# Kernel tuning notes

Hardware: AMD Instinct MI355X
Metric: run time of the kernel (lower is better)

Reference implementation:

```python
import jax, jax.numpy as jnp
import numpy as np

N = 8192        # batch rows
D = 1024        # final_dim (power of 2, == init_dim so padding = 0)
STACK = 4       # nbr_stack
SIGMA = 1.0


def _hadamard(n):
    H = np.array([[1.0]], dtype=np.float32)
    while H.shape[0] < n:
        H = np.block([[H, H], [H, -H]])
    return H


def setup_inputs() -> dict:
    key = jax.random.key(0)
    x = jax.random.normal(key, (N, D), dtype=jnp.float32)
    rs = np.random.RandomState(0)
    # B: random signs (diag), shape (STACK, D)
    B = jnp.asarray(rs.choice([-1.0, 1.0], size=(STACK, D)).astype(np.float32))
    # G: gaussian diag, flattened to (STACK*D,)
    G2 = rs.randn(STACK, D).astype(np.float32)
    G = jnp.asarray(G2.reshape(STACK * D))
    # S: chi-like scaling normalized by per-stack norm of G, flattened
    G_norm = np.linalg.norm(G2, axis=1, keepdims=True)
    S2 = (np.abs(rs.randn(STACK, D)).astype(np.float32) * np.sqrt(D)) / G_norm
    S = jnp.asarray(S2.reshape(STACK * D).astype(np.float32))
    # H: dense Walsh-Hadamard matrix (D, D), +-1 entries (non-trainable constant)
    H = jnp.asarray(_hadamard(D))
    # P: per-stack permutation with stack offsets, gathered along feature axis
    P = jnp.asarray(np.concatenate([rs.permutation(D) + i * D for i in range(STACK)]).astype(np.int32))
    bias = jnp.zeros((2 * STACK * D,), dtype=jnp.float32)
    return {"x": x, "B": B, "G": G, "S": S, "bias": bias, "H": H, "P": P}


def reference(x, B, G, S, bias, H, P):
    n = x.shape[0]
    # padding = final_dim - init_dim = 0 here; pad kept for faithfulness
    xp = jnp.pad(x.reshape(-1, D), ((0, 0), (0, 0)))
    # diag B then Hadamard matmul: [n, STACK, D]
    h = xp[:, None, :] * B
    h = jnp.einsum('nsd,de->nse', h, H).reshape(n, STACK * D)
    # permutation gather, diag G
    h = h[:, P] * G
    # second Hadamard matmul
    h = jnp.einsum('nsd,de->nse', h.reshape(n, STACK, D), H).reshape(n, STACK * D)
    # scale by 1/(sigma*sqrt(D)) and diag S
    h = (1.0 / (SIGMA * np.sqrt(D))) * h * S
    # cos/sin random-feature activation
    out = np.sqrt(1.0 / D).astype(np.float32) * jnp.concatenate([jnp.cos(h), jnp.sin(h)], axis=1)
    out = out + bias
    return out
```

## Files before the change

### kernel.cpp

```cpp
#include <hip/hip_runtime.h>
#include <math.h>


#define FF_D 1024
#define FF_STACK 4
#define FF_NT 256

__device__ __forceinline__ int swz(int e) { return e ^ (((e >> 6) & 7) << 2); }

#define STAGE_BIT(vv, m) { \
    _Pragma("unroll") \
    for (int i_ = 0; i_ < 16; ++i_) \
        if (!(i_ & (m))) { \
            float s_ = vv[i_] + vv[i_ | (m)]; \
            float d_ = vv[i_] - vv[i_ | (m)]; \
            vv[i_] = s_; vv[i_ | (m)] = d_; \
        } \
}

__global__ __launch_bounds__(FF_NT) void fastfood_kernel(
    const float* __restrict__ x,
    const float* __restrict__ Bs,
    const float* __restrict__ G,
    const float* __restrict__ S,
    const float* __restrict__ bias,
    const int*   __restrict__ P,
    float* __restrict__ out)
{
    __shared__ float lds[FF_STACK * FF_D];
    const int lane = threadIdx.x & 63;
    const int s    = threadIdx.x >> 6;
    const int row  = blockIdx.x;
    const int sb   = s << 10;
    float* wl = lds + sb;

    const int eB = (lane & 3) | ((lane & 60) << 4);
    const float kout = 0.03125f;
    const float karg = 0.03125f * 0.15915494309f;

    float v[16];

    #pragma unroll
    for (int q = 0; q < 4; ++q) {
        const float4 t  = *(const float4*)&x[((long long)row << 10) + (q << 8) + (lane << 2)];
        const float4 b4 = *(const float4*)&Bs[sb + (q << 8) + (lane << 2)];
        v[4*q+0] = t.x * b4.x; v[4*q+1] = t.y * b4.y;
        v[4*q+2] = t.z * b4.z; v[4*q+3] = t.w * b4.w;
    }

    STAGE_BIT(v, 1) STAGE_BIT(v, 2) STAGE_BIT(v, 4) STAGE_BIT(v, 8)
    #pragma unroll
    for (int q = 0; q < 4; ++q)
        *(float4*)&wl[swz((q << 8) | (lane << 2))] =
            make_float4(v[4*q], v[4*q+1], v[4*q+2], v[4*q+3]);
    __builtin_amdgcn_wave_barrier();
    #pragma unroll
    for (int r = 0; r < 16; ++r) v[r] = wl[swz(eB | (r << 2))];
    STAGE_BIT(v, 1) STAGE_BIT(v, 2) STAGE_BIT(v, 4) STAGE_BIT(v, 8)
    __builtin_amdgcn_wave_barrier();
    #pragma unroll
    for (int r = 0; r < 16; ++r) wl[swz(eB | (r << 2))] = v[r];
    __builtin_amdgcn_wave_barrier();
    #pragma unroll
    for (int q = 0; q < 4; ++q) {
        const float4 t = *(const float4*)&wl[swz(((lane & 15) << 2) | (q << 6) | ((lane & 48) << 4))];
        v[4*q+0] = t.x; v[4*q+1] = t.y; v[4*q+2] = t.z; v[4*q+3] = t.w;
    }
    STAGE_BIT(v, 4) STAGE_BIT(v, 8)

    __builtin_amdgcn_wave_barrier();
    #pragma unroll
    for (int q = 0; q < 4; ++q)
        *(float4*)&wl[swz(((lane & 15) << 2) | (q << 6) | ((lane & 48) << 4))] =
            make_float4(v[4*q], v[4*q+1], v[4*q+2], v[4*q+3]);
    __builtin_amdgcn_wave_barrier();
    #pragma unroll
    for (int q = 0; q < 4; ++q) {
        const int jb = sb + (q << 8) + (lane << 2);
        const int4   p4 = *(const int4*)&P[jb];
        const float4 g4 = *(const float4*)&G[jb];
        v[4*q+0] = wl[swz(p4.x & (FF_D - 1))] * g4.x;
        v[4*q+1] = wl[swz(p4.y & (FF_D - 1))] * g4.y;
        v[4*q+2] = wl[swz(p4.z & (FF_D - 1))] * g4.z;
        v[4*q+3] = wl[swz(p4.w & (FF_D - 1))] * g4.w;
    }

    STAGE_BIT(v, 1) STAGE_BIT(v, 2) STAGE_BIT(v, 4) STAGE_BIT(v, 8)
    __builtin_amdgcn_wave_barrier();
    #pragma unroll
    for (int q = 0; q < 4; ++q)
        *(float4*)&wl[swz((q << 8) | (lane << 2))] =
            make_float4(v[4*q], v[4*q+1], v[4*q+2], v[4*q+3]);
    __builtin_amdgcn_wave_barrier();
    #pragma unroll
    for (int r = 0; r < 16; ++r) v[r] = wl[swz(eB | (r << 2))];
    STAGE_BIT(v, 1) STAGE_BIT(v, 2) STAGE_BIT(v, 4) STAGE_BIT(v, 8)
    __builtin_amdgcn_wave_barrier();
    #pragma unroll
    for (int r = 0; r < 16; ++r) wl[swz(eB | (r << 2))] = v[r];
    __builtin_amdgcn_wave_barrier();
    #pragma unroll
    for (int q = 0; q < 4; ++q) {
        const float4 t = *(const float4*)&wl[swz(((lane & 15) << 2) | (q << 6) | ((lane & 48) << 4))];
        v[4*q+0] = t.x; v[4*q+1] = t.y; v[4*q+2] = t.z; v[4*q+3] = t.w;
    }
    STAGE_BIT(v, 4) STAGE_BIT(v, 8)

    const long long obase = ((long long)row << 13);
    #pragma unroll
    for (int q = 0; q < 4; ++q) {
        const int e0 = ((lane & 15) << 2) | (q << 6) | ((lane & 48) << 4);
        const int j  = sb + e0;
        const float4 s4  = *(const float4*)&S[j];
        const float4 bc4 = *(const float4*)&bias[j];
        const float4 bs4 = *(const float4*)&bias[FF_STACK * FF_D + j];
        float4 oc, os;
        {
            const float tr = __builtin_amdgcn_fractf(v[4*q+0] * (s4.x * karg));
            oc.x = __builtin_amdgcn_cosf(tr) * kout + bc4.x;
            os.x = __builtin_amdgcn_sinf(tr) * kout + bs4.x;
        }
        {
            const float tr = __builtin_amdgcn_fractf(v[4*q+1] * (s4.y * karg));
            oc.y = __builtin_amdgcn_cosf(tr) * kout + bc4.y;
            os.y = __builtin_amdgcn_sinf(tr) * kout + bs4.y;
        }
        {
            const float tr = __builtin_amdgcn_fractf(v[4*q+2] * (s4.z * karg));
            oc.z = __builtin_amdgcn_cosf(tr) * kout + bc4.z;
            os.z = __builtin_amdgcn_sinf(tr) * kout + bs4.z;
        }
        {
            const float tr = __builtin_amdgcn_fractf(v[4*q+3] * (s4.w * karg));
            oc.w = __builtin_amdgcn_cosf(tr) * kout + bc4.w;
            os.w = __builtin_amdgcn_sinf(tr) * kout + bs4.w;
        }
        *(float4*)&out[obase + j] = oc;
        *(float4*)&out[obase + FF_STACK * FF_D + j] = os;
    }
}

extern "C" void kernel_launch(void* const* d_in, const int* in_sizes, int n_in,
                              void* d_out, int out_size, void* d_ws, size_t ws_size,
                              hipStream_t stream) {
    const float* x    = (const float*)d_in[0];
    const float* B    = (const float*)d_in[1];
    const float* G    = (const float*)d_in[2];
    const float* S    = (const float*)d_in[3];
    const float* bias = (const float*)d_in[4];
    const int*   P    = (const int*)d_in[6];
    float* out = (float*)d_out;

    const int n_rows = in_sizes[0] / FF_D;
    fastfood_kernel<<<n_rows, FF_NT, 0, stream>>>(x, B, G, S, bias, P, out);
}
```

Measured before the change: 321.1 us.

## Replace LDS transposes in Hadamard transform with cross-lane swizzle butterflies

The LDS store/load transposes used for the upper butterfly stages of each 1024-point Walsh-Hadamard transform are replaced. Those stages now run as cross-lane exchanges (ds_swizzle for lane distances 1-16, shfl_xor for 32), with a per-lane sign applied through an FMA. LDS is kept only for the permutation gather, now without address swizzling. This removes LDS round trips and wave barriers but issues 16 swizzle ops per stage across 6 stages, and the unswizzled gather may hit more bank conflicts.

```diff
diff --git a/kernel.cpp b/kernel.cpp
--- a/kernel.cpp
+++ b/kernel.cpp
@@ -1,12 +1,12 @@
 #include <hip/hip_runtime.h>
-#include <math.h>
 
 
 #define FF_D 1024
 #define FF_STACK 4
 #define FF_NT 256
 
-__device__ __forceinline__ int swz(int e) { return e ^ (((e >> 6) & 7) << 2); }
+#define SWZF(vf, OFF) \
+    __int_as_float(__builtin_amdgcn_ds_swizzle(__float_as_int(vf), (OFF)))
 
 #define STAGE_BIT(vv, m) { \
     _Pragma("unroll") \
@@ -16,6 +16,32 @@
             float d_ = vv[i_] - vv[i_ | (m)]; \
             vv[i_] = s_; vv[i_ | (m)] = d_; \
         } \
+}
+
+#define STAGE_SWZ(vv, OFF, sgn) { \
+    float p_[16]; \
+    _Pragma("unroll") \
+    for (int i_ = 0; i_ < 16; ++i_) p_[i_] = SWZF(vv[i_], OFF); \
+    _Pragma("unroll") \
+    for (int i_ = 0; i_ < 16; ++i_) vv[i_] = __builtin_fmaf(sgn, vv[i_], p_[i_]); \
+}
+
+#define STAGE_X32(vv, sgn) { \
+    float p_[16]; \
+    _Pragma("unroll") \
+    for (int i_ = 0; i_ < 16; ++i_) p_[i_] = __shfl_xor(vv[i_], 32, 64); \
+    _Pragma("unroll") \
+    for (int i_ = 0; i_ < 16; ++i_) vv[i_] = __builtin_fmaf(sgn, vv[i_], p_[i_]); \
+}
+
+#define FWHT10(vv) { \
+    STAGE_BIT(vv, 1) STAGE_BIT(vv, 2) STAGE_BIT(vv, 4) STAGE_BIT(vv, 8) \
+    STAGE_SWZ(vv, 0x041F, sg1)   \
+    STAGE_SWZ(vv, 0x081F, sg2)   \
+    STAGE_SWZ(vv, 0x101F, sg4)   \
+    STAGE_SWZ(vv, 0x201F, sg8)   \
+    STAGE_SWZ(vv, 0x401F, sg16)  \
+    STAGE_X32(vv, sg32)          \
 }
 
 __global__ __launch_bounds__(FF_NT) void fastfood_kernel(
@@ -34,7 +60,13 @@
     const int sb   = s << 10;
     float* wl = lds + sb;
 
-    const int eB = (lane & 3) | ((lane & 60) << 4);
+    const float sg1  = (lane & 1)  ? -1.0f : 1.0f;
+    const float sg2  = (lane & 2)  ? -1.0f : 1.0f;
+    const float sg4  = (lane & 4)  ? -1.0f : 1.0f;
+    const float sg8  = (lane & 8)  ? -1.0f : 1.0f;
+    const float sg16 = (lane & 16) ? -1.0f : 1.0f;
+    const float sg32 = (lane & 32) ? -1.0f : 1.0f;
+
     const float kout = 0.03125f;
     const float karg = 0.03125f * 0.15915494309f;
 
@@ -48,30 +80,11 @@
         v[4*q+2] = t.z * b4.z; v[4*q+3] = t.w * b4.w;
     }
 
-    STAGE_BIT(v, 1) STAGE_BIT(v, 2) STAGE_BIT(v, 4) STAGE_BIT(v, 8)
+    FWHT10(v)
+
     #pragma unroll
     for (int q = 0; q < 4; ++q)
-        *(float4*)&wl[swz((q << 8) | (lane << 2))] =
-            make_float4(v[4*q], v[4*q+1], v[4*q+2], v[4*q+3]);
-    __builtin_amdgcn_wave_barrier();
-    #pragma unroll
-    for (int r = 0; r < 16; ++r) v[r] = wl[swz(eB | (r << 2))];
-    STAGE_BIT(v, 1) STAGE_BIT(v, 2) STAGE_BIT(v, 4) STAGE_BIT(v, 8)
-    __builtin_amdgcn_wave_barrier();
-    #pragma unroll
-    for (int r = 0; r < 16; ++r) wl[swz(eB | (r << 2))] = v[r];
-    __builtin_amdgcn_wave_barrier();
-    #pragma unroll
-    for (int q = 0; q < 4; ++q) {
-        const float4 t = *(const float4*)&wl[swz(((lane & 15) << 2) | (q << 6) | ((lane & 48) << 4))];
-        v[4*q+0] = t.x; v[4*q+1] = t.y; v[4*q+2] = t.z; v[4*q+3] = t.w;
-    }
-    STAGE_BIT(v, 4) STAGE_BIT(v, 8)
-
-    __builtin_amdgcn_wave_barrier();
-    #pragma unroll
-    for (int q = 0; q < 4; ++q)
-        *(float4*)&wl[swz(((lane & 15) << 2) | (q << 6) | ((lane & 48) << 4))] =
+        *(float4*)&wl[(q << 8) | (lane << 2)] =
             make_float4(v[4*q], v[4*q+1], v[4*q+2], v[4*q+3]);
     __builtin_amdgcn_wave_barrier();
     #pragma unroll
@@ -79,38 +92,18 @@
         const int jb = sb + (q << 8) + (lane << 2);
         const int4   p4 = *(const int4*)&P[jb];
         const float4 g4 = *(const float4*)&G[jb];
-        v[4*q+0] = wl[swz(p4.x & (FF_D - 1))] * g4.x;
-        v[4*q+1] = wl[swz(p4.y & (FF_D - 1))] * g4.y;
-        v[4*q+2] = wl[swz(p4.z & (FF_D - 1))] * g4.z;
-        v[4*q+3] = wl[swz(p4.w & (FF_D - 1))] * g4.w;
+        v[4*q+0] = wl[p4.x & (FF_D - 1)] * g4.x;
+        v[4*q+1] = wl[p4.y & (FF_D - 1)] * g4.y;
+        v[4*q+2] = wl[p4.z & (FF_D - 1)] * g4.z;
+        v[4*q+3] = wl[p4.w & (FF_D - 1)] * g4.w;
     }
 
-    STAGE_BIT(v, 1) STAGE_BIT(v, 2) STAGE_BIT(v, 4) STAGE_BIT(v, 8)
-    __builtin_amdgcn_wave_barrier();
-    #pragma unroll
-    for (int q = 0; q < 4; ++q)
-        *(float4*)&wl[swz((q << 8) | (lane << 2))] =
-            make_float4(v[4*q], v[4*q+1], v[4*q+2], v[4*q+3]);
-    __builtin_amdgcn_wave_barrier();
-    #pragma unroll
-    for (int r = 0; r < 16; ++r) v[r] = wl[swz(eB | (r << 2))];
-    STAGE_BIT(v, 1) STAGE_BIT(v, 2) STAGE_BIT(v, 4) STAGE_BIT(v, 8)
-    __builtin_amdgcn_wave_barrier();
-    #pragma unroll
-    for (int r = 0; r < 16; ++r) wl[swz(eB | (r << 2))] = v[r];
-    __builtin_amdgcn_wave_barrier();
-    #pragma unroll
-    for (int q = 0; q < 4; ++q) {
-        const float4 t = *(const float4*)&wl[swz(((lane & 15) << 2) | (q << 6) | ((lane & 48) << 4))];
-        v[4*q+0] = t.x; v[4*q+1] = t.y; v[4*q+2] = t.z; v[4*q+3] = t.w;
-    }
-    STAGE_BIT(v, 4) STAGE_BIT(v, 8)
+    FWHT10(v)
 
     const long long obase = ((long long)row << 13);
     #pragma unroll
     for (int q = 0; q < 4; ++q) {
-        const int e0 = ((lane & 15) << 2) | (q << 6) | ((lane & 48) << 4);
-        const int j  = sb + e0;
+        const int j = sb + (q << 8) + (lane << 2);
         const float4 s4  = *(const float4*)&S[j];
         const float4 bc4 = *(const float4*)&bias[j];
         const float4 bs4 = *(const float4*)&bias[FF_STACK * FF_D + j];
```

Result: no change. 326.3 us (+1.6%).
